# Kernel tuning notes

Hardware: AMD Instinct MI355X
Metric: run time of the kernel (lower is better)

The kernel has to match this reference:

```python
import jax, jax.numpy as jnp
import numpy as np

N_EMBD = 1024
N_HEAD = 16
HEAD_SIZE = N_EMBD // N_HEAD
D_FF = 4 * N_EMBD
B, T = 4, 2048
EPS = 1e-5


def _layernorm(x, w, b):
    mu = jnp.mean(x, axis=-1, keepdims=True)
    var = jnp.mean(jnp.square(x - mu), axis=-1, keepdims=True)
    return (x - mu) * jax.lax.rsqrt(var + EPS) * w + b


def setup_inputs() -> dict:
    key = jax.random.key(0)
    ks = jax.random.split(key, 12)
    s = 0.02
    x = jax.random.normal(ks[0], (B, T, N_EMBD), dtype=jnp.float32)
    # right-padded prefix mask: lengths in [T//2, T] -> no all-masked causal rows
    lengths = jax.random.randint(ks[1], (B,), T // 2, T + 1)
    key_padding_mask = jnp.arange(T)[None, :] < lengths[:, None]  # [B,T] bool, True=keep
    wq = jax.random.normal(ks[2], (N_EMBD, N_HEAD, HEAD_SIZE), dtype=jnp.float32) * s
    wk = jax.random.normal(ks[3], (N_EMBD, N_HEAD, HEAD_SIZE), dtype=jnp.float32) * s
    wv = jax.random.normal(ks[4], (N_EMBD, N_HEAD, HEAD_SIZE), dtype=jnp.float32) * s
    proj_w = jax.random.normal(ks[5], (N_EMBD, N_EMBD), dtype=jnp.float32) * s
    proj_b = jnp.zeros((N_EMBD,), dtype=jnp.float32)
    ff_w1 = jax.random.normal(ks[6], (N_EMBD, D_FF), dtype=jnp.float32) * s
    ff_b1 = jnp.zeros((D_FF,), dtype=jnp.float32)
    ff_w2 = jax.random.normal(ks[7], (D_FF, N_EMBD), dtype=jnp.float32) * s
    ff_b2 = jnp.zeros((N_EMBD,), dtype=jnp.float32)
    ln1_w = jnp.ones((N_EMBD,), dtype=jnp.float32)
    ln1_b = jnp.zeros((N_EMBD,), dtype=jnp.float32)
    ln2_w = jnp.ones((N_EMBD,), dtype=jnp.float32)
    ln2_b = jnp.zeros((N_EMBD,), dtype=jnp.float32)
    return dict(x=x, key_padding_mask=key_padding_mask, wq=wq, wk=wk, wv=wv,
                proj_w=proj_w, proj_b=proj_b, ff_w1=ff_w1, ff_b1=ff_b1,
                ff_w2=ff_w2, ff_b2=ff_b2, ln1_w=ln1_w, ln1_b=ln1_b,
                ln2_w=ln2_w, ln2_b=ln2_b)


def reference(x, key_padding_mask, wq, wk, wv, proj_w, proj_b,
              ff_w1, ff_b1, ff_w2, ff_b2, ln1_w, ln1_b, ln2_w, ln2_b):
    Bn, Tn, C = x.shape
    m = key_padding_mask.astype(x.dtype)  # [B,T]
    # --- attention sublayer ---
    h = _layernorm(x, ln1_w, ln1_b) * m[..., None]
    q = jnp.einsum('btc,chd->bhtd', h, wq)
    k = jnp.einsum('btc,chd->bhtd', h, wk)
    v = jnp.einsum('btc,chd->bhtd', h, wv)
    # NOTE: original scales by full embed dim C**-0.5, not head_size
    scores = jnp.einsum('bhtd,bhsd->bhts', q, k) * (C ** -0.5)
    causal = jnp.tril(jnp.ones((Tn, Tn), dtype=bool))
    mask = causal[None, None, :, :] & key_padding_mask[:, None, None, :]
    scores = jnp.where(mask, scores, -jnp.inf)
    wei = jax.nn.softmax(scores, axis=-1)
    out = jnp.einsum('bhts,bhsd->bthd', wei, v).reshape(Bn, Tn, C)
    x = x + out @ proj_w + proj_b
    # --- feedforward sublayer ---
    h2 = _layernorm(x, ln2_w, ln2_b) * m[..., None]
    ff = jax.nn.relu(h2 @ ff_w1 + ff_b1) @ ff_w2 + ff_b2
    x = (x + ff) * m[..., None]
    return x
```

## Files before the change

### kernel.cpp

```cpp
#include <hip/hip_runtime.h>
#include <math.h>

typedef float f32x4 __attribute__((ext_vector_type(4)));
typedef float f4 __attribute__((ext_vector_type(4)));
typedef __bf16 bf16x8 __attribute__((ext_vector_type(8)));
typedef __bf16 bf16x4 __attribute__((ext_vector_type(4)));

#define GLOBAL_AS __attribute__((address_space(1)))
#define LDS_AS __attribute__((address_space(3)))

__global__ __launch_bounds__(256) void mask_canon(const unsigned char* __restrict__ raw,
                                                  float* __restrict__ msk, int n) {
    int i = blockIdx.x * 256 + threadIdx.x;
    if (i >= n) return;
    unsigned int w0 = *(const unsigned int*)raw;
    float v;
    if (w0 == 0x01010101u)       v = raw[i] ? 1.f : 0.f;
    else if (w0 == 0x3f800000u)  v = ((const float*)raw)[i];
    else                         v = ((const int*)raw)[i] ? 1.f : 0.f;
    msk[i] = v;
}

__global__ __launch_bounds__(256) void lens_kernel(const float* __restrict__ msk,
                                                   float* __restrict__ lens) {
    int b = blockIdx.x, tid = threadIdx.x;
    float s = 0.f;
    for (int i = tid; i < 2048; i += 256) s += msk[b * 2048 + i];
#pragma unroll
    for (int off = 1; off < 64; off <<= 1) s += __shfl_xor(s, off);
    __shared__ float red[4];
    int wave = tid >> 6, lane = tid & 63;
    if (lane == 0) red[wave] = s;
    __syncthreads();
    if (tid == 0) lens[b] = red[0] + red[1] + red[2] + red[3];
}

__global__ __launch_bounds__(256) void tcvt(const float* __restrict__ src,
                                            __bf16* __restrict__ dst, int K, int N) {
    __shared__ float tile[32][33];
    int n0 = blockIdx.x * 32, k0 = blockIdx.y * 32;
    int tx = threadIdx.x & 31, ty = threadIdx.x >> 5;
#pragma unroll
    for (int i = 0; i < 4; ++i)
        tile[ty + 8 * i][tx] = src[(long)(k0 + ty + 8 * i) * N + n0 + tx];
    __syncthreads();
#pragma unroll
    for (int i = 0; i < 4; ++i)
        dst[(long)(n0 + ty + 8 * i) * K + k0 + tx] = (__bf16)tile[tx][ty + 8 * i];
}

__global__ __launch_bounds__(256) void ln_kernel(const float* __restrict__ x,
                                                 const float* __restrict__ w,
                                                 const float* __restrict__ bsc,
                                                 const float* __restrict__ msk,
                                                 __bf16* __restrict__ out) {
    long row = blockIdx.x;
    int tid = threadIdx.x;
    f4 xv = *(const f4*)(x + row * 1024 + tid * 4);
    float s = xv[0] + xv[1] + xv[2] + xv[3];
    float sq = xv[0] * xv[0] + xv[1] * xv[1] + xv[2] * xv[2] + xv[3] * xv[3];
#pragma unroll
    for (int off = 1; off < 64; off <<= 1) {
        s += __shfl_xor(s, off);
        sq += __shfl_xor(sq, off);
    }
    __shared__ float red[2][4];
    int wave = tid >> 6, lane = tid & 63;
    if (lane == 0) { red[0][wave] = s; red[1][wave] = sq; }
    __syncthreads();
    s = red[0][0] + red[0][1] + red[0][2] + red[0][3];
    sq = red[1][0] + red[1][1] + red[1][2] + red[1][3];
    float mu = s * (1.0f / 1024.0f);
    float var = sq * (1.0f / 1024.0f) - mu * mu;
    float rs = rsqrtf(var + 1e-5f);
    float mv = msk[row];
    f4 wv = *(const f4*)(w + tid * 4);
    f4 bv = *(const f4*)(bsc + tid * 4);
    bf16x4 ov;
#pragma unroll
    for (int j = 0; j < 4; ++j)
        ov[j] = (__bf16)(((xv[j] - mu) * rs * wv[j] + bv[j]) * mv);
    *(bf16x4*)(out + row * 1024 + tid * 4) = ov;
}

template <int EP>
__global__ __launch_bounds__(256) void gemm_bt(const __bf16* __restrict__ A,
                                               const __bf16* __restrict__ B,
                                               int K, int N, void* __restrict__ Cout,
                                               const float* __restrict__ bias,
                                               const float* __restrict__ resid,
                                               const float* __restrict__ mskp) {
    __shared__ __bf16 As[128 * 32];
    __shared__ __bf16 Bs[128 * 32];
    int tid = threadIdx.x;
    int wave = tid >> 6, lane = tid & 63;
    int l15 = lane & 15, quad = lane >> 4;
    int wrow = (wave >> 1) * 64, wcol = (wave & 1) * 64;
    long rowBase = (long)blockIdx.x * 128;
    long colBase = (long)blockIdx.y * 128;
    const __bf16* Ab = A + rowBase * K;
    const __bf16* Bb = B + colBase * K;
    int srow = lane >> 2;
    int scol = (lane & 3) * 8;
    f32x4 acc[4][4] = {};

    for (int kt = 0; kt < K; kt += 32) {
#pragma unroll
        for (int j = 0; j < 2; ++j) {
            int seg = wave * 2 + j;
            const __bf16* ga = Ab + (long)(seg * 16 + srow) * K + kt + scol;
            const __bf16* gb = Bb + (long)(seg * 16 + srow) * K + kt + scol;
            __builtin_amdgcn_global_load_lds((const GLOBAL_AS void*)ga,
                                             (LDS_AS void*)((char*)As + seg * 1024), 16, 0, 0);
            __builtin_amdgcn_global_load_lds((const GLOBAL_AS void*)gb,
                                             (LDS_AS void*)((char*)Bs + seg * 1024), 16, 0, 0);
        }
        __syncthreads();
        bf16x8 af[4], bfr[4];
#pragma unroll
        for (int i = 0; i < 4; ++i) {
            af[i] = *(const bf16x8*)(As + (wrow + i * 16 + l15) * 32 + quad * 8);
            bfr[i] = *(const bf16x8*)(Bs + (wcol + i * 16 + l15) * 32 + quad * 8);
        }
#pragma unroll
        for (int mi = 0; mi < 4; ++mi)
#pragma unroll
            for (int ni = 0; ni < 4; ++ni)
                acc[mi][ni] = __builtin_amdgcn_mfma_f32_16x16x32_bf16(af[mi], bfr[ni], acc[mi][ni], 0, 0, 0);
        __syncthreads();
    }

#pragma unroll
    for (int mi = 0; mi < 4; ++mi) {
#pragma unroll
        for (int r = 0; r < 4; ++r) {
            long gr = rowBase + wrow + mi * 16 + quad * 4 + r;
#pragma unroll
            for (int ni = 0; ni < 4; ++ni) {
                long gc = colBase + wcol + ni * 16 + l15;
                float v = acc[mi][ni][r];
                if constexpr (EP == 0) {
                    ((__bf16*)Cout)[gr * N + gc] = (__bf16)v;
                } else if constexpr (EP == 1) {
                    v += bias[gc];
                    v = v > 0.f ? v : 0.f;
                    ((__bf16*)Cout)[gr * N + gc] = (__bf16)v;
                } else if constexpr (EP == 2) {
                    v += bias[gc] + resid[gr * N + gc];
                    ((float*)Cout)[gr * N + gc] = v;
                } else {
                    v = (v + bias[gc] + resid[gr * N + gc]) * mskp[gr];
                    ((float*)Cout)[gr * N + gc] = v;
                }
            }
        }
    }
}

#define SWIZ(row, d) ((row) * 64 + ((((d) >> 3) ^ ((row) & 7)) << 3) + ((d) & 7))
__global__ __launch_bounds__(256, 3) void attn_kernel(const __bf16* __restrict__ qkv,
                                                      const float* __restrict__ lens,
                                                      __bf16* __restrict__ att) {
    const int T = 2048, C3 = 3072;
    int bh = blockIdx.x;
    int qt = 15 - blockIdx.y;
    int h = bh & 15, b = bh >> 4;
    int tid = threadIdx.x;
    int wave = tid >> 6, lane = tid & 63, l15 = lane & 15, quad = lane >> 4;

    __shared__ __bf16 Kl[64 * 64];
    __shared__ __bf16 Vt[64 * 64];
    __shared__ __bf16 Pl[4][32 * 64];

    long rowB = (long)b * T;
    const __bf16* kbase = qkv + rowB * C3 + 1024 + h * 64;
    const __bf16* vbase = qkv + rowB * C3 + 2048 + h * 64;
    const float scale2 = (1.0f / 32.0f) * 1.44269504088896f;

    int krow = tid >> 2, kd = (tid & 3) * 16;
    int vk = (tid & 15) * 4, vd = (tid >> 4) * 4;
    int vc8 = vk >> 3, vk7 = vk & 7;

    bf16x8 ones;
#pragma unroll
    for (int j = 0; j < 8; ++j) ones[j] = (__bf16)1.0f;

    __bf16* pw = &Pl[wave][0];
    int r8 = l15 & 7;

    int qbase = qt * 128;
    int wq0 = qbase + wave * 32;

    bf16x8 qf[2][2];
#pragma unroll
    for (int g = 0; g < 2; ++g) {
        const __bf16* qptr = qkv + (rowB + wq0 + g * 16 + l15) * C3 + h * 64;
        qf[g][0] = *(const bf16x8*)(qptr + quad * 8);
        qf[g][1] = *(const bf16x8*)(qptr + 32 + quad * 8);
    }

    f32x4 o0[4] = {}, o1[4] = {};
    f32x4 lacc0 = {}, lacc1 = {};
    int nchunk = 2 * qt + 2;
    float len = lens[b];

    bf16x8 kpre0, kpre1;
    bf16x4 vpre[4];
    {
        const __bf16* kg = kbase + (long)krow * C3 + kd;
        kpre0 = *(const bf16x8*)kg;
        kpre1 = *(const bf16x8*)(kg + 8);
#pragma unroll
        for (int j = 0; j < 4; ++j)
            vpre[j] = *(const bf16x4*)(vbase + (long)(vk + j) * C3 + vd);
    }

    for (int c = 0; c < nchunk; ++c) {
        int k0 = c * 64;
        __asm__ volatile("s_barrier" ::: "memory");
        *(bf16x8*)(&Kl[SWIZ(krow, kd)]) = kpre0;
        *(bf16x8*)(&Kl[SWIZ(krow, kd + 8)]) = kpre1;
#pragma unroll
        for (int dd = 0; dd < 4; ++dd) {
            bf16x4 w = {vpre[0][dd], vpre[1][dd], vpre[2][dd], vpre[3][dd]};
            int d = vd + dd;
            *(bf16x4*)(&Vt[d * 64 + ((vc8 ^ (d & 7)) << 3) + vk7]) = w;
        }
        if (c + 1 < nchunk) {
            int k1 = k0 + 64;
            const __bf16* kg = kbase + (long)(k1 + krow) * C3 + kd;
            kpre0 = *(const bf16x8*)kg;
            kpre1 = *(const bf16x8*)(kg + 8);
#pragma unroll
            for (int j = 0; j < 4; ++j)
                vpre[j] = *(const bf16x4*)(vbase + (long)(k1 + vk + j) * C3 + vd);
        }
        __asm__ volatile("s_waitcnt lgkmcnt(0)\n\ts_barrier" ::: "memory");

        if (k0 <= wq0 + 31) {
            f32x4 s0[4] = {}, s1[4] = {};
#pragma unroll
            for (int n = 0; n < 4; ++n) {
                int row = n * 16 + l15;
                bf16x8 kb0 = *(const bf16x8*)(&Kl[row * 64 + ((quad ^ r8) << 3)]);
                bf16x8 kb1 = *(const bf16x8*)(&Kl[row * 64 + (((4 + quad) ^ r8) << 3)]);
                s0[n] = __builtin_amdgcn_mfma_f32_16x16x32_bf16(kb0, qf[0][0], s0[n], 0, 0, 0);
                s0[n] = __builtin_amdgcn_mfma_f32_16x16x32_bf16(kb1, qf[0][1], s0[n], 0, 0, 0);
                s1[n] = __builtin_amdgcn_mfma_f32_16x16x32_bf16(kb0, qf[1][0], s1[n], 0, 0, 0);
                s1[n] = __builtin_amdgcn_mfma_f32_16x16x32_bf16(kb1, qf[1][1], s1[n], 0, 0, 0);
            }

            bool needC = (k0 + 63 > wq0);
#pragma unroll
            for (int n = 0; n < 4; ++n) {
                int c8 = n * 2 + (quad >> 1);
                int sub = (quad & 1) * 4;
                bf16x4 w0, w1;
                if (!needC) {
#pragma unroll
                    for (int r = 0; r < 4; ++r) {
                        w0[r] = (__bf16)exp2f(s0[n][r] * scale2);
                        w1[r] = (__bf16)exp2f(s1[n][r] * scale2);
                    }
                } else {
                    int kg = k0 + n * 16 + quad * 4;
                    int qg0 = wq0 + l15, qg1 = wq0 + 16 + l15;
#pragma unroll
                    for (int r = 0; r < 4; ++r) {
                        w0[r] = (kg + r <= qg0) ? (__bf16)exp2f(s0[n][r] * scale2) : (__bf16)0.f;
                        w1[r] = (kg + r <= qg1) ? (__bf16)exp2f(s1[n][r] * scale2) : (__bf16)0.f;
                    }
                }
                int wbase = l15 * 64 + ((c8 ^ r8) << 3) + sub;
                *(bf16x4*)(pw + wbase) = w0;
                *(bf16x4*)(pw + 1024 + wbase) = w1;
            }
            __asm__ volatile("s_waitcnt lgkmcnt(0)" ::: "memory");

            bf16x8 pa00 = *(const bf16x8*)(pw + l15 * 64 + ((quad ^ r8) << 3));
            bf16x8 pa01 = *(const bf16x8*)(pw + l15 * 64 + (((4 + quad) ^ r8) << 3));
            bf16x8 pa10 = *(const bf16x8*)(pw + 1024 + l15 * 64 + ((quad ^ r8) << 3));
            bf16x8 pa11 = *(const bf16x8*)(pw + 1024 + l15 * 64 + (((4 + quad) ^ r8) << 3));
#pragma unroll
            for (int nd = 0; nd < 4; ++nd) {
                int row = nd * 16 + l15;
                bf16x8 vb0 = *(const bf16x8*)(&Vt[row * 64 + ((quad ^ r8) << 3)]);
                bf16x8 vb1 = *(const bf16x8*)(&Vt[row * 64 + (((4 + quad) ^ r8) << 3)]);
                o0[nd] = __builtin_amdgcn_mfma_f32_16x16x32_bf16(pa00, vb0, o0[nd], 0, 0, 0);
                o0[nd] = __builtin_amdgcn_mfma_f32_16x16x32_bf16(pa01, vb1, o0[nd], 0, 0, 0);
                o1[nd] = __builtin_amdgcn_mfma_f32_16x16x32_bf16(pa10, vb0, o1[nd], 0, 0, 0);
                o1[nd] = __builtin_amdgcn_mfma_f32_16x16x32_bf16(pa11, vb1, o1[nd], 0, 0, 0);
            }
            lacc0 = __builtin_amdgcn_mfma_f32_16x16x32_bf16(pa00, ones, lacc0, 0, 0, 0);
            lacc0 = __builtin_amdgcn_mfma_f32_16x16x32_bf16(pa01, ones, lacc0, 0, 0, 0);
            lacc1 = __builtin_amdgcn_mfma_f32_16x16x32_bf16(pa10, ones, lacc1, 0, 0, 0);
            lacc1 = __builtin_amdgcn_mfma_f32_16x16x32_bf16(pa11, ones, lacc1, 0, 0, 0);
        }
    }

#pragma unroll
    for (int r = 0; r < 4; ++r) {
        int q0g = wq0 + quad * 4 + r;
        float inv0 = 1.0f / (lacc0[r] - fmaxf(0.f, (float)(q0g + 1) - len));
        long orow0 = rowB + q0g;
        int q1g = q0g + 16;
        float inv1 = 1.0f / (lacc1[r] - fmaxf(0.f, (float)(q1g + 1) - len));
        long orow1 = rowB + q1g;
#pragma unroll
        for (int nd = 0; nd < 4; ++nd) {
            att[orow0 * 1024 + h * 64 + nd * 16 + l15] = (__bf16)(o0[nd][r] * inv0);
            att[orow1 * 1024 + h * 64 + nd * 16 + l15] = (__bf16)(o1[nd][r] * inv1);
        }
    }
}

extern "C" void kernel_launch(void* const* d_in, const int* in_sizes, int n_in,
                              void* d_out, int out_size, void* d_ws, size_t ws_size,
                              hipStream_t stream) {
    const float* x      = (const float*)d_in[0];
    const void*  kpm    = d_in[1];
    const float* wq     = (const float*)d_in[2];
    const float* wk     = (const float*)d_in[3];
    const float* wv     = (const float*)d_in[4];
    const float* proj_w = (const float*)d_in[5];
    const float* proj_b = (const float*)d_in[6];
    const float* ff_w1  = (const float*)d_in[7];
    const float* ff_b1  = (const float*)d_in[8];
    const float* ff_w2  = (const float*)d_in[9];
    const float* ff_b2  = (const float*)d_in[10];
    const float* ln1w   = (const float*)d_in[11];
    const float* ln1b   = (const float*)d_in[12];
    const float* ln2w   = (const float*)d_in[13];
    const float* ln2b   = (const float*)d_in[14];

    char* ws = (char*)d_ws;
    size_t off = 0;
    auto take = [&](size_t bytes) -> char* {
        char* p = ws + off;
        off += (bytes + 255) & ~(size_t)255;
        return p;
    };
    float*  msk    = (float*)take(8192 * 4);
    float*  lens   = (float*)take(256);
    __bf16* wqkvT  = (__bf16*)take(3072L * 1024 * 2);
    __bf16* wprojT = (__bf16*)take(1024L * 1024 * 2);
    __bf16* wff1T  = (__bf16*)take(4096L * 1024 * 2);
    __bf16* wff2T  = (__bf16*)take(4096L * 1024 * 2);
    __bf16* h1     = (__bf16*)take(8192L * 1024 * 2);
    char*   qkv_c  = take(8192L * 3072 * 2);
    __bf16* qkvb   = (__bf16*)qkv_c;
    __bf16* attb   = (__bf16*)take(8192L * 1024 * 2);
    float*  x2     = (float*)take(8192L * 1024 * 4);
    __bf16* h2     = (__bf16*)take(8192L * 1024 * 2);
    __bf16* ffh    = (__bf16*)qkv_c;

    mask_canon<<<32, 256, 0, stream>>>((const unsigned char*)kpm, msk, 8192);
    lens_kernel<<<4, 256, 0, stream>>>(msk, lens);
    tcvt<<<dim3(32, 32), 256, 0, stream>>>(wq, wqkvT, 1024, 1024);
    tcvt<<<dim3(32, 32), 256, 0, stream>>>(wk, wqkvT + 1024L * 1024, 1024, 1024);
    tcvt<<<dim3(32, 32), 256, 0, stream>>>(wv, wqkvT + 2048L * 1024, 1024, 1024);
    tcvt<<<dim3(32, 32), 256, 0, stream>>>(proj_w, wprojT, 1024, 1024);
    tcvt<<<dim3(128, 32), 256, 0, stream>>>(ff_w1, wff1T, 1024, 4096);
    tcvt<<<dim3(32, 128), 256, 0, stream>>>(ff_w2, wff2T, 4096, 1024);

    ln_kernel<<<8192, 256, 0, stream>>>(x, ln1w, ln1b, msk, h1);
    gemm_bt<0><<<dim3(64, 24), 256, 0, stream>>>(h1, wqkvT, 1024, 3072, qkvb, nullptr, nullptr, nullptr);
    attn_kernel<<<dim3(64, 16), 256, 0, stream>>>(qkvb, lens, attb);
    gemm_bt<2><<<dim3(64, 8), 256, 0, stream>>>(attb, wprojT, 1024, 1024, x2, proj_b, x, nullptr);
    ln_kernel<<<8192, 256, 0, stream>>>(x2, ln2w, ln2b, msk, h2);
    gemm_bt<1><<<dim3(64, 32), 256, 0, stream>>>(h2, wff1T, 1024, 4096, ffh, ff_b1, nullptr, nullptr);
    gemm_bt<3><<<dim3(64, 8), 256, 0, stream>>>(ffh, wff2T, 4096, 1024, (float*)d_out, ff_b2, x2, msk);
}
```

Before: 544.8 us.

## Add 256x256-tile 8-wave pipelined GEMM for QKV and FF1 projections

Introduces a new GEMM kernel with 512 threads and 256x256 output tiles, double-buffered LDS filled via direct global-to-LDS loads, with the next tile's loads interleaved between MFMA phases and raised wave priority during matrix ops. It replaces the 128x128 GEMM for the QKV and FF1 projections to increase data reuse per block and overlap memory with compute. The larger tile leaves fewer blocks (384 and 512) and more register and LDS pressure per block, which risks lower occupancy and tail imbalance across the CUs.

Result: faster. 497.4 us (-8.7%).

```diff
diff --git a/kernel.cpp b/kernel.cpp
--- a/kernel.cpp
+++ b/kernel.cpp
@@ -139,18 +139,134 @@
             for (int ni = 0; ni < 4; ++ni) {
                 long gc = colBase + wcol + ni * 16 + l15;
                 float v = acc[mi][ni][r];
-                if constexpr (EP == 0) {
-                    ((__bf16*)Cout)[gr * N + gc] = (__bf16)v;
-                } else if constexpr (EP == 1) {
-                    v += bias[gc];
-                    v = v > 0.f ? v : 0.f;
-                    ((__bf16*)Cout)[gr * N + gc] = (__bf16)v;
-                } else if constexpr (EP == 2) {
+                if constexpr (EP == 2) {
                     v += bias[gc] + resid[gr * N + gc];
                     ((float*)Cout)[gr * N + gc] = v;
                 } else {
                     v = (v + bias[gc] + resid[gr * N + gc]) * mskp[gr];
                     ((float*)Cout)[gr * N + gc] = v;
+                }
+            }
+        }
+    }
+}
+
+template <int EP>
+__global__ __launch_bounds__(512, 2) void gemm_bt8(const __bf16* __restrict__ A,
+                                                   const __bf16* __restrict__ B,
+                                                   int K, int N, void* __restrict__ Cout,
+                                                   const float* __restrict__ bias) {
+    __shared__ __bf16 AB[2][2][256 * 64];
+    int tid = threadIdx.x;
+    int wave = tid >> 6, lane = tid & 63;
+    int l15 = lane & 15, quad = lane >> 4;
+    int r8 = l15 & 7;
+    int wm = wave >> 2, wn = wave & 3;
+    long rowBase = (long)blockIdx.x * 256;
+    long colBase = (long)blockIdx.y * 256;
+    const __bf16* Ab = A + rowBase * K;
+    const __bf16* Bb = B + colBase * K;
+    int srow = lane >> 3;
+    int scol = ((lane & 7) ^ srow) * 8;
+    f32x4 acc[8][4] = {};
+
+#define STAGE2(DST, GB, seg0, kt_)                                                         \
+    do {                                                                                   \
+        _Pragma("unroll") for (int j = 0; j < 2; ++j) {                                    \
+            int s_ = wave * 4 + (seg0) + j;                                                \
+            const __bf16* g_ = (GB) + (long)(s_ * 8 + srow) * K + (kt_) + scol;            \
+            __builtin_amdgcn_global_load_lds((const GLOBAL_AS void*)g_,                    \
+                                             (LDS_AS void*)((char*)(DST) + s_ * 1024), 16, \
+                                             0, 0);                                        \
+        }                                                                                  \
+    } while (0)
+
+#define RDA(mh)                                                                      \
+    do {                                                                             \
+        _Pragma("unroll") for (int mi = 0; mi < 4; ++mi) {                           \
+            int row_ = wm * 128 + (mh) * 64 + mi * 16 + l15;                         \
+            af[mi][0] = *(const bf16x8*)(Ac + row_ * 64 + ((quad ^ r8) << 3));       \
+            af[mi][1] = *(const bf16x8*)(Ac + row_ * 64 + (((4 + quad) ^ r8) << 3)); \
+        }                                                                            \
+    } while (0)
+
+#define RDB(h)                                                                              \
+    do {                                                                                    \
+        _Pragma("unroll") for (int ni = 0; ni < 2; ++ni) {                                  \
+            int row_ = wn * 64 + ((h) * 2 + ni) * 16 + l15;                                 \
+            bfr[h][ni][0] = *(const bf16x8*)(Bc + row_ * 64 + ((quad ^ r8) << 3));          \
+            bfr[h][ni][1] = *(const bf16x8*)(Bc + row_ * 64 + (((4 + quad) ^ r8) << 3));    \
+        }                                                                                   \
+    } while (0)
+
+#define MM(mh, nh)                                                                          \
+    do {                                                                                    \
+        __builtin_amdgcn_s_setprio(1);                                                      \
+        _Pragma("unroll") for (int mi = 0; mi < 4; ++mi) {                                  \
+            _Pragma("unroll") for (int ni = 0; ni < 2; ++ni) {                              \
+                acc[(mh) * 4 + mi][(nh) * 2 + ni] = __builtin_amdgcn_mfma_f32_16x16x32_bf16(\
+                    af[mi][0], bfr[nh][ni][0], acc[(mh) * 4 + mi][(nh) * 2 + ni], 0, 0, 0); \
+                acc[(mh) * 4 + mi][(nh) * 2 + ni] = __builtin_amdgcn_mfma_f32_16x16x32_bf16(\
+                    af[mi][1], bfr[nh][ni][1], acc[(mh) * 4 + mi][(nh) * 2 + ni], 0, 0, 0); \
+            }                                                                               \
+        }                                                                                   \
+        __builtin_amdgcn_s_setprio(0);                                                      \
+    } while (0)
+
+    STAGE2(&AB[0][0][0], Ab, 0, 0);
+    STAGE2(&AB[0][0][0], Ab, 2, 0);
+    STAGE2(&AB[0][1][0], Bb, 0, 0);
+    STAGE2(&AB[0][1][0], Bb, 2, 0);
+
+    int cur = 0;
+    bf16x8 af[4][2], bfr[2][2][2];
+    for (int kt = 0; kt < K; kt += 64) {
+        const bool lastt = (kt + 64 >= K);
+        const __bf16* Ac = &AB[cur][0][0];
+        const __bf16* Bc = &AB[cur][1][0];
+        __bf16* An = &AB[cur ^ 1][0][0];
+        __bf16* Bn = &AB[cur ^ 1][1][0];
+        if (!lastt) {
+            STAGE2(An, Ab, 0, kt + 64);
+            __asm__ volatile("s_waitcnt vmcnt(2)" ::: "memory");
+        } else {
+            __asm__ volatile("s_waitcnt vmcnt(0)" ::: "memory");
+        }
+        __asm__ volatile("s_barrier" ::: "memory");
+        RDA(0);
+        RDB(0);
+        MM(0, 0);
+        if (!lastt) STAGE2(An, Ab, 2, kt + 64);
+        RDB(1);
+        MM(0, 1);
+        if (!lastt) STAGE2(Bn, Bb, 0, kt + 64);
+        RDA(1);
+        MM(1, 1);
+        if (!lastt) STAGE2(Bn, Bb, 2, kt + 64);
+        MM(1, 0);
+        __asm__ volatile("s_barrier" ::: "memory");
+        cur ^= 1;
+    }
+#undef STAGE2
+#undef RDA
+#undef RDB
+#undef MM
+
+#pragma unroll
+    for (int mi = 0; mi < 8; ++mi) {
+#pragma unroll
+        for (int r = 0; r < 4; ++r) {
+            long gr = rowBase + wm * 128 + mi * 16 + quad * 4 + r;
+#pragma unroll
+            for (int ni = 0; ni < 4; ++ni) {
+                long gc = colBase + wn * 64 + ni * 16 + l15;
+                float v = acc[mi][ni][r];
+                if constexpr (EP == 0) {
+                    ((__bf16*)Cout)[gr * N + gc] = (__bf16)v;
+                } else {
+                    v += bias[gc];
+                    v = v > 0.f ? v : 0.f;
+                    ((__bf16*)Cout)[gr * N + gc] = (__bf16)v;
                 }
             }
         }
@@ -364,10 +480,10 @@
     tcvt<<<dim3(32, 128), 256, 0, stream>>>(ff_w2, wff2T, 4096, 1024);
 
     ln_kernel<<<8192, 256, 0, stream>>>(x, ln1w, ln1b, msk, h1);
-    gemm_bt<0><<<dim3(64, 24), 256, 0, stream>>>(h1, wqkvT, 1024, 3072, qkvb, nullptr, nullptr, nullptr);
+    gemm_bt8<0><<<dim3(32, 12), 512, 0, stream>>>(h1, wqkvT, 1024, 3072, qkvb, nullptr);
     attn_kernel<<<dim3(64, 16), 256, 0, stream>>>(qkvb, lens, attb);
     gemm_bt<2><<<dim3(64, 8), 256, 0, stream>>>(attb, wprojT, 1024, 1024, x2, proj_b, x, nullptr);
     ln_kernel<<<8192, 256, 0, stream>>>(x2, ln2w, ln2b, msk, h2);
-    gemm_bt<1><<<dim3(64, 32), 256, 0, stream>>>(h2, wff1T, 1024, 4096, ffh, ff_b1, nullptr, nullptr);
+    gemm_bt8<1><<<dim3(32, 16), 512, 0, stream>>>(h2, wff1T, 1024, 4096, ffh, ff_b1);
     gemm_bt<3><<<dim3(64, 8), 256, 0, stream>>>(ffh, wff2T, 4096, 1024, (float*)d_out, ff_b2, x2, msk);
 }
```
